# Performance work log

Hardware: AMD Instinct MI355X
Metric: run time of the kernel (lower is better)

The kernel has to match this reference:

```python
import jax, jax.numpy as jnp
import numpy as np

B, L, D, H, DH, DEPTH, VOCAB = 8, 512, 256, 8, 64, 16, 5
INNER = 4 * D  # GLU feedforward inner dim = 1024
EPS = 1e-5

def _ln(x, g, b):
    mu = jnp.mean(x, -1, keepdims=True)
    var = jnp.mean(jnp.square(x - mu), -1, keepdims=True)
    return (x - mu) * jax.lax.rsqrt(var + EPS) * g + b

def setup_inputs() -> dict:
    key = jax.random.key(0)
    ks = jax.random.split(key, 24)
    s = 0.02
    seq = jax.random.randint(ks[0], (B, L), 0, VOCAB)
    lengths = jax.random.randint(ks[1], (B,), L // 2, L + 1)
    mask = jnp.arange(L)[None, :] < lengths[:, None]  # [B, L] bool padding mask
    f32 = jnp.float32
    return {
        "seq": seq,
        "mask": mask,
        "emb": jax.random.normal(ks[2], (VOCAB, D), f32) * s,
        "png": jnp.ones((D,), f32), "pnb": jnp.zeros((D,), f32),
        "ln1g": jnp.ones((DEPTH, D), f32), "ln1b": jnp.zeros((DEPTH, D), f32),
        "Wq": jax.random.normal(ks[3], (DEPTH, D, H * DH), f32) * s,
        "Wk": jax.random.normal(ks[4], (DEPTH, D, H * DH), f32) * s,
        "Wv": jax.random.normal(ks[5], (DEPTH, D, H * DH), f32) * s,
        "Wo": jax.random.normal(ks[6], (DEPTH, H * DH, D), f32) * s,
        "ln2g": jnp.ones((DEPTH, D), f32), "ln2b": jnp.zeros((DEPTH, D), f32),
        "W1": jax.random.normal(ks[7], (DEPTH, D, 2 * INNER), f32) * s,
        "b1": jnp.zeros((DEPTH, 2 * INNER), f32),
        "W2": jax.random.normal(ks[8], (DEPTH, INNER, D), f32) * s,
        "b2": jnp.zeros((DEPTH, D), f32),
        "fng": jnp.ones((D,), f32), "fnb": jnp.zeros((D,), f32),
        "Wout": jax.random.normal(ks[9], (D, 2), f32) * s,
        "bout": jnp.zeros((2,), f32),
    }

def _alibi_bias(n):
    # heads=8 is a power of two: slopes = 2^{-1}..2^{-8}
    slopes = 2.0 ** (-(jnp.arange(1, H + 1, dtype=jnp.float32)) * (8.0 / H))
    pos = jnp.arange(n, dtype=jnp.float32)
    rel = -jnp.abs(pos[None, :] - pos[:, None])  # [n, n]
    return slopes[:, None, None] * rel  # [H, n, n]

def _forward(seq, mask, emb, png, pnb, ln1g, ln1b, Wq, Wk, Wv, Wo,
             ln2g, ln2b, W1, b1, W2, b2, fng, fnb, Wout, bout):
    x = emb[seq]                      # [B, L, D]
    x = _ln(x, png, pnb)              # post_emb_norm
    bias = _alibi_bias(L)             # [H, L, L]
    kv_mask = mask[:, None, None, :]  # [B, 1, 1, L]
    scale = DH ** -0.5

    def layer(x, p):
        (g1, c1, wq, wk, wv, wo, g2, c2, w1, bb1, w2, bb2) = p
        h = _ln(x, g1, c1)
        q = (h @ wq).reshape(B, L, H, DH).transpose(0, 2, 1, 3)  # bhld
        k = (h @ wk).reshape(B, L, H, DH).transpose(0, 2, 1, 3)
        v = (h @ wv).reshape(B, L, H, DH).transpose(0, 2, 1, 3)
        scores = jnp.einsum('bhid,bhjd->bhij', q, k) * scale + bias
        scores = jnp.where(kv_mask, scores, jnp.float32(-1e9))
        a = jax.nn.softmax(scores, axis=-1)
        o = jnp.einsum('bhij,bhjd->bhid', a, v)
        o = o.transpose(0, 2, 1, 3).reshape(B, L, H * DH) @ wo
        x = x + o
        h2 = _ln(x, g2, c2)
        u = h2 @ w1 + bb1
        val, gate = jnp.split(u, 2, axis=-1)  # GLU: x * gelu(gate)
        x = x + (val * jax.nn.gelu(gate, approximate=False)) @ w2 + bb2
        return x, None

    x, _ = jax.lax.scan(layer, x, (ln1g, ln1b, Wq, Wk, Wv, Wo, ln2g, ln2b, W1, b1, W2, b2))
    x = _ln(x, fng, fnb)              # final encoder norm
    return x @ Wout + bout            # [B, L, 2]

def reference(seq, mask, emb, png, pnb, ln1g, ln1b, Wq, Wk, Wv, Wo,
              ln2g, ln2b, W1, b1, W2, b2, fng, fnb, Wout, bout):
    return _forward(seq, mask, emb, png, pnb, ln1g, ln1b, Wq, Wk, Wv, Wo,
                    ln2g, ln2b, W1, b1, W2, b2, fng, fnb, Wout, bout)
```

## Files before the change

### kernel.cpp

```cpp
#include <hip/hip_runtime.h>
#include <cstdint>
#include <cstddef>

#define BB 8
#define LL 512
#define DD 256
#define HH 8
#define DHD 64
#define NLAYER 16
#define HDH 512
#define IN2 2048
#define IN1 1024

typedef __attribute__((ext_vector_type(8))) short short8;
typedef __attribute__((ext_vector_type(4))) float floatx4;
typedef __attribute__((ext_vector_type(4))) unsigned short ushort4v;
typedef unsigned short u16;

__device__ __forceinline__ floatx4 mfma16(short8 a, short8 b, floatx4 c) {
  return __builtin_amdgcn_mfma_f32_16x16x32_bf16(a, b, c, 0, 0, 0);
}

__device__ __forceinline__ u16 f2b(float f) {
  union { float f; unsigned u; } x; x.f = f;
  unsigned u = x.u + 0x7fffu + ((x.u >> 16) & 1u);
  return (u16)(u >> 16);
}
__device__ __forceinline__ float b2f(u16 s) {
  union { unsigned u; float f; } x; x.u = ((unsigned)s) << 16;
  return x.f;
}

__device__ __forceinline__ float wave_sum(float s) {
#pragma unroll
  for (int off = 32; off; off >>= 1) s += __shfl_xor(s, off);
  return s;
}

__device__ __forceinline__ void gload_lds16(const u16* g, u16* l) {
  __builtin_amdgcn_global_load_lds((__attribute__((address_space(1))) void*)g,
                                   (__attribute__((address_space(3))) void*)l,
                                   16, 0, 0);
}

template <int NSLOTS>
__device__ __forceinline__ void stage_tile(const u16* __restrict__ g, int rowstride,
                                           u16* lds, int tid) {
  int wave = tid >> 6, lane = tid & 63;
#pragma unroll
  for (int j = 0; j < NSLOTS / 256; ++j) {
    int sbase = j * 256 + wave * 64;
    int slot = sbase + lane;
    int row = slot >> 3;
    int kg = (slot & 7) ^ (row & 7);
    gload_lds16(g + (size_t)row * rowstride + kg * 8, lds + sbase * 8);
  }
}

__device__ __forceinline__ short8 ld_frag(const u16* T, int row, int kg) {
  return *(const short8*)&T[(row << 6) + (((kg ^ row) & 7) << 3)];
}

__device__ __forceinline__ float4 ln_math(const float* __restrict__ x,
                                          const float* __restrict__ g,
                                          const float* __restrict__ b, int t) {
  float4 v = *(const float4*)(x + t * 4);
  float s = wave_sum(v.x + v.y + v.z + v.w);
  float mu = s * (1.0f / DD);
  float dx = v.x - mu, dy = v.y - mu, dz = v.z - mu, dw = v.w - mu;
  float ss = wave_sum(dx * dx + dy * dy + dz * dz + dw * dw);
  float r = rsqrtf(ss * (1.0f / DD) + 1e-5f);
  float4 gg = *(const float4*)(g + t * 4);
  float4 bb = *(const float4*)(b + t * 4);
  float4 o;
  o.x = dx * r * gg.x + bb.x;
  o.y = dy * r * gg.y + bb.y;
  o.z = dz * r * gg.z + bb.z;
  o.w = dw * r * gg.w + bb.w;
  return o;
}

__global__ __launch_bounds__(256) void embed_ln_kernel(
    const int* __restrict__ seq, const float* __restrict__ emb,
    const float* __restrict__ png, const float* __restrict__ pnb,
    const float* __restrict__ g1, const float* __restrict__ b1,
    float* __restrict__ X, u16* __restrict__ H) {
  int row = blockIdx.x * 4 + (threadIdx.x >> 6), t = threadIdx.x & 63;
  int tok = seq[row];
  float4 o = ln_math(emb + (size_t)tok * DD, png, pnb, t);
  *(float4*)(X + (size_t)row * DD + t * 4) = o;
  float s = wave_sum(o.x + o.y + o.z + o.w);
  float mu = s * (1.0f / DD);
  float dx = o.x - mu, dy = o.y - mu, dz = o.z - mu, dw = o.w - mu;
  float ss = wave_sum(dx * dx + dy * dy + dz * dz + dw * dw);
  float r = rsqrtf(ss * (1.0f / DD) + 1e-5f);
  float4 gg = *(const float4*)(g1 + t * 4);
  float4 bb = *(const float4*)(b1 + t * 4);
  ushort4v o4;
  o4[0] = f2b(dx * r * gg.x + bb.x);
  o4[1] = f2b(dy * r * gg.y + bb.y);
  o4[2] = f2b(dz * r * gg.z + bb.z);
  o4[3] = f2b(dw * r * gg.w + bb.w);
  *(ushort4v*)(H + (size_t)row * DD + t * 4) = o4;
}

#define WBUF_LAYER 1310720
__global__ __launch_bounds__(256) void prep_weights_kernel(
    const float* __restrict__ Wq, const float* __restrict__ Wk,
    const float* __restrict__ Wv, const float* __restrict__ Wo,
    const float* __restrict__ W1, const float* __restrict__ W2,
    u16* __restrict__ wbuf_all) {
  __shared__ float tile[32][33];
  int l = blockIdx.x / 1280;
  int bx = blockIdx.x % 1280;
  int tid = threadIdx.x;
  const float* wq = Wq + (size_t)l * DD * HDH;
  const float* wk = Wk + (size_t)l * DD * HDH;
  const float* wv = Wv + (size_t)l * DD * HDH;
  const float* wo = Wo + (size_t)l * HDH * DD;
  const float* w1 = W1 + (size_t)l * DD * IN2;
  const float* w2 = W2 + (size_t)l * IN1 * DD;
  u16* wbuf = wbuf_all + (size_t)l * WBUF_LAYER;

  const float* src; int srcld; u16* dst; int dstld; int dn0, k0, scol0;
  int packW1 = 0;
  if (bx < 384) {
    int t = bx; dn0 = (t % 48) * 32; k0 = (t / 48) * 32;
    scol0 = dn0 & 511;
    src = (dn0 < 512) ? wq : ((dn0 < 1024) ? wk : wv);
    srcld = 512; dst = wbuf; dstld = 256;
  } else if (bx < 512) {
    int t = bx - 384; dn0 = (t % 8) * 32; k0 = (t / 8) * 32; scol0 = dn0;
    src = wo; srcld = 256; dst = wbuf + 393216; dstld = 512;
  } else if (bx < 1024) {
    int t = bx - 512; dn0 = (t % 64) * 32; k0 = (t / 64) * 32; scol0 = dn0;
    src = w1; srcld = 2048; dst = wbuf + 524288; dstld = 256; packW1 = 1;
  } else {
    int t = bx - 1024; dn0 = (t % 8) * 32; k0 = (t / 8) * 32; scol0 = dn0;
    src = w2; srcld = 256; dst = wbuf + 1048576; dstld = 1024;
  }
  int r = tid >> 3, c4 = (tid & 7) * 4;
  float4 v = *(const float4*)&src[(size_t)(k0 + r) * srcld + scol0 + c4];
  tile[r][c4 + 0] = v.x; tile[r][c4 + 1] = v.y;
  tile[r][c4 + 2] = v.z; tile[r][c4 + 3] = v.w;
  __syncthreads();
  int n = tid >> 3, kk = (tid & 7) * 4;
  int drow = dn0 + n;
  if (packW1) {
    if (drow < 1024) drow = ((drow >> 4) << 5) | (drow & 15);
    else { int nn = drow - 1024; drow = (((nn >> 4) << 5) + 16) | (nn & 15); }
  }
  ushort4v o4;
  o4[0] = f2b(tile[kk + 0][n]); o4[1] = f2b(tile[kk + 1][n]);
  o4[2] = f2b(tile[kk + 2][n]); o4[3] = f2b(tile[kk + 3][n]);
  *(ushort4v*)&dst[(size_t)drow * dstld + k0 + kk] = o4;
}

__global__ __launch_bounds__(256) void gemm_qkv(
    const u16* __restrict__ A, const u16* __restrict__ BT,
    u16* __restrict__ qk, u16* __restrict__ vT) {
  __shared__ __align__(16) u16 As[128 * 64];
  __shared__ __align__(16) u16 Bs[128 * 64];
  int tid = threadIdx.x;
  int wave = tid >> 6, lane = tid & 63;
  int lm = lane & 15, quad = lane >> 4;
  int wr = wave >> 1, wc = wave & 1;
  int n0 = blockIdx.x * 128, m0 = blockIdx.y * 128;

  floatx4 acc[4][4];
#pragma unroll
  for (int mf = 0; mf < 4; ++mf)
#pragma unroll
    for (int nf = 0; nf < 4; ++nf)
#pragma unroll
      for (int r = 0; r < 4; ++r) acc[mf][nf][r] = 0.0f;

  for (int k0 = 0; k0 < DD; k0 += 64) {
    __syncthreads();
    stage_tile<1024>(A + (size_t)m0 * DD + k0, DD, As, tid);
    stage_tile<1024>(BT + (size_t)n0 * DD + k0, DD, Bs, tid);
    __syncthreads();
#pragma unroll
    for (int kc = 0; kc < 2; ++kc) {
      short8 af[4], bf[4];
#pragma unroll
      for (int mf = 0; mf < 4; ++mf)
        af[mf] = ld_frag(As, wr * 64 + mf * 16 + lm, kc * 4 + quad);
#pragma unroll
      for (int nf = 0; nf < 4; ++nf)
        bf[nf] = ld_frag(Bs, wc * 64 + nf * 16 + lm, kc * 4 + quad);
#pragma unroll
      for (int mf = 0; mf < 4; ++mf)
#pragma unroll
        for (int nf = 0; nf < 4; ++nf)
          acc[mf][nf] = mfma16(af[mf], bf[nf], acc[mf][nf]);
    }
  }
  if (n0 < 1024) {
#pragma unroll
    for (int mf = 0; mf < 4; ++mf)
#pragma unroll
      for (int nf = 0; nf < 4; ++nf)
#pragma unroll
        for (int r = 0; r < 4; ++r) {
          int row = m0 + wr * 64 + mf * 16 + quad * 4 + r;
          int col = n0 + wc * 64 + nf * 16 + lm;
          qk[(size_t)row * 1024 + col] = f2b(acc[mf][nf][r]);
        }
  } else {
#pragma unroll
    for (int mf = 0; mf < 4; ++mf)
#pragma unroll
      for (int nf = 0; nf < 4; ++nf) {
        int token0 = m0 + wr * 64 + mf * 16 + quad * 4;
        int hd = n0 + wc * 64 + nf * 16 + lm - 1024;
        int b = token0 >> 9, key = token0 & 511;
        ushort4v p4;
#pragma unroll
        for (int r = 0; r < 4; ++r) p4[r] = f2b(acc[mf][nf][r]);
        *(ushort4v*)&vT[((size_t)(b * 8 + (hd >> 6)) * 64 + (hd & 63)) * 512 + key] = p4;
      }
  }
}

__global__ __launch_bounds__(256) void gemm_ffn1(
    const u16* __restrict__ A, const u16* __restrict__ BTp,
    const float* __restrict__ b1, u16* __restrict__ G) {
  __shared__ __align__(16) u16 As[128 * 64];
  __shared__ __align__(16) u16 Bs[128 * 64];
  int tid = threadIdx.x;
  int wave = tid >> 6, lane = tid & 63;
  int lm = lane & 15, quad = lane >> 4;
  int wr = wave >> 1, wc = wave & 1;
  int n0 = blockIdx.x * 128, m0 = blockIdx.y * 128;

  floatx4 acc[4][4];
#pragma unroll
  for (int mf = 0; mf < 4; ++mf)
#pragma unroll
    for (int nf = 0; nf < 4; ++nf)
#pragma unroll
      for (int r = 0; r < 4; ++r) acc[mf][nf][r] = 0.0f;

  for (int k0 = 0; k0 < DD; k0 += 64) {
    __syncthreads();
    stage_tile<1024>(A + (size_t)m0 * DD + k0, DD, As, tid);
    stage_tile<1024>(BTp + (size_t)n0 * DD + k0, DD, Bs, tid);
    __syncthreads();
#pragma unroll
    for (int kc = 0; kc < 2; ++kc) {
      short8 af[4], bf[4];
#pragma unroll
      for (int mf = 0; mf < 4; ++mf)
        af[mf] = ld_frag(As, wr * 64 + mf * 16 + lm, kc * 4 + quad);
#pragma unroll
      for (int nf = 0; nf < 4; ++nf)
        bf[nf] = ld_frag(Bs, wc * 64 + nf * 16 + lm, kc * 4 + quad);
#pragma unroll
      for (int mf = 0; mf < 4; ++mf)
#pragma unroll
        for (int nf = 0; nf < 4; ++nf)
          acc[mf][nf] = mfma16(af[mf], bf[nf], acc[mf][nf]);
    }
  }
  int p0 = (n0 + wc * 64) >> 5;
#pragma unroll
  for (int j = 0; j < 2; ++j) {
    int gcol = (p0 + j) * 16 + lm;
    float bv = b1[gcol], bg = b1[1024 + gcol];
#pragma unroll
    for (int mf = 0; mf < 4; ++mf)
#pragma unroll
      for (int r = 0; r < 4; ++r) {
        int row = m0 + wr * 64 + mf * 16 + quad * 4 + r;
        float val = acc[mf][2 * j][r] + bv;
        float gate = acc[mf][2 * j + 1][r] + bg;
        float ge = 0.5f * gate * (1.0f + erff(gate * 0.70710678118654752440f));
        G[(size_t)row * IN1 + gcol] = f2b(val * ge);
      }
  }
}

__global__ __launch_bounds__(256) void gemm_row_ln(
    const u16* __restrict__ A, int lda, const u16* __restrict__ BT, int K,
    const float* __restrict__ bias, float* __restrict__ X,
    const float* __restrict__ lng, const float* __restrict__ lnb,
    u16* __restrict__ Hout) {
  __shared__ __align__(16) u16 As[16 * 64];
  __shared__ __align__(16) u16 Bs[256 * 64];
  int tid = threadIdx.x;
  int wave = tid >> 6, lane = tid & 63;
  int lm = lane & 15, quad = lane >> 4;
  int m0 = blockIdx.x * 16;

  floatx4 acc[4];
#pragma unroll
  for (int nf = 0; nf < 4; ++nf)
#pragma unroll
    for (int r = 0; r < 4; ++r) acc[nf][r] = 0.0f;

  for (int k0 = 0; k0 < K; k0 += 64) {
    __syncthreads();
    if (wave < 2) {
      int sbase = wave * 64;
      int slot = sbase + lane;
      int row = slot >> 3;
      int kg = (slot & 7) ^ (row & 7);
      gload_lds16(A + (size_t)(m0 + row) * lda + k0 + kg * 8, As + sbase * 8);
    }
    stage_tile<2048>(BT + k0, K, Bs, tid);
    __syncthreads();
#pragma unroll
    for (int kc = 0; kc < 2; ++kc) {
      short8 af = ld_frag(As, lm, kc * 4 + quad);
#pragma unroll
      for (int nf = 0; nf < 4; ++nf) {
        short8 bf = ld_frag(Bs, wave * 64 + nf * 16 + lm, kc * 4 + quad);
        acc[nf] = mfma16(af, bf, acc[nf]);
      }
    }
  }
  __syncthreads();
  float* xs = (float*)Bs;
#pragma unroll
  for (int nf = 0; nf < 4; ++nf) {
    int col = wave * 64 + nf * 16 + lm;
    float bv = bias ? bias[col] : 0.0f;
#pragma unroll
    for (int r = 0; r < 4; ++r) {
      int row = quad * 4 + r;
      float v = acc[nf][r] + bv + X[(size_t)(m0 + row) * DD + col];
      X[(size_t)(m0 + row) * DD + col] = v;
      xs[row * DD + col] = v;
    }
  }
  __syncthreads();
  float4 gg = *(const float4*)(lng + lane * 4);
  float4 bb = *(const float4*)(lnb + lane * 4);
#pragma unroll
  for (int rr = 0; rr < 4; ++rr) {
    int row = wave * 4 + rr;
    float4 v = *(const float4*)&xs[row * DD + lane * 4];
    float s = wave_sum(v.x + v.y + v.z + v.w);
    float mu = s * (1.0f / DD);
    float dx = v.x - mu, dy = v.y - mu, dz = v.z - mu, dw = v.w - mu;
    float ss = wave_sum(dx * dx + dy * dy + dz * dz + dw * dw);
    float rc = rsqrtf(ss * (1.0f / DD) + 1e-5f);
    ushort4v o4;
    o4[0] = f2b(dx * rc * gg.x + bb.x);
    o4[1] = f2b(dy * rc * gg.y + bb.y);
    o4[2] = f2b(dz * rc * gg.z + bb.z);
    o4[3] = f2b(dw * rc * gg.w + bb.w);
    *(ushort4v*)(Hout + (size_t)(m0 + row) * DD + lane * 4) = o4;
  }
}

__global__ __launch_bounds__(256) void attn_mfma_kernel(
    const u16* __restrict__ qk, const u16* __restrict__ vT,
    const int* __restrict__ mask_raw, u16* __restrict__ O) {
  __shared__ __align__(16) u16 Ks[64 * 64];
  __shared__ __align__(16) u16 Vs[64 * 64];
  __shared__ __align__(16) u16 Ps[4][16][72];
  __shared__ __align__(16) float madd[64];

  const int tid = threadIdx.x, wave = tid >> 6, lane = tid & 63;
  const int lm = lane & 15, quad = lane >> 4;
  const int qb = blockIdx.x, h = blockIdx.y, b = blockIdx.z;
  const float slope = exp2f(-(float)(h + 1));

  int w0 = mask_raw[0];
  int mmode = (w0 == 1) ? 0 : ((w0 == 0x3f800000) ? 2 : 1);

  const int q0 = qb * 64 + wave * 16;
  const int qg = b * LL + q0;
  const float qpos = (float)(q0 + lm);

  const u16* qp = qk + (size_t)(qg + lm) * 1024 + h * 64 + quad * 8;
  short8 qf0 = *(const short8*)qp;
  short8 qf1 = *(const short8*)(qp + 32);

  floatx4 oc[4];
#pragma unroll
  for (int nf = 0; nf < 4; ++nf)
#pragma unroll
    for (int r = 0; r < 4; ++r) oc[nf][r] = 0.0f;
  float mrow = -1e30f, lrow = 0.0f;

  const int krow_base = b * LL;
  const u16* vbase = vT + (size_t)(b * 8 + h) * 64 * 512;
  for (int k0 = 0; k0 < LL; k0 += 64) {
    bool tile_valid;
    if (mmode == 0) tile_valid = mask_raw[krow_base + k0] != 0;
    else if (mmode == 1) tile_valid = ((const signed char*)mask_raw)[krow_base + k0] != 0;
    else tile_valid = ((const float*)mask_raw)[krow_base + k0] != 0.0f;
    if (!tile_valid) break;

    __syncthreads();
    stage_tile<512>(qk + (size_t)(krow_base + k0) * 1024 + 512 + h * 64, 1024, Ks, tid);
    stage_tile<512>(vbase + k0, 512, Vs, tid);
    if (tid < 64) {
      int gi = krow_base + k0 + tid;
      bool valid;
      if (mmode == 0) valid = mask_raw[gi] != 0;
      else if (mmode == 1) valid = ((const signed char*)mask_raw)[gi] != 0;
      else valid = ((const float*)mask_raw)[gi] != 0.0f;
      madd[tid] = valid ? 0.0f : -1e9f;
    }
    __syncthreads();

    float sc[4][4];
    float tmax = -3e38f;
#pragma unroll
    for (int nt = 0; nt < 4; ++nt) {
      floatx4 pc;
#pragma unroll
      for (int r = 0; r < 4; ++r) pc[r] = 0.0f;
      short8 kf0 = ld_frag(Ks, nt * 16 + lm, quad);
      short8 kf1 = ld_frag(Ks, nt * 16 + lm, 4 + quad);
      pc = mfma16(kf0, qf0, pc);
      pc = mfma16(kf1, qf1, pc);
      float4 ma = *(const float4*)&madd[nt * 16 + quad * 4];
      float kbase = (float)(k0 + nt * 16 + quad * 4);
#pragma unroll
      for (int r = 0; r < 4; ++r) {
        float s = pc[r] * 0.125f - slope * fabsf(qpos - (kbase + r)) +
                  ((const float*)&ma)[r];
        sc[nt][r] = s;
        tmax = fmaxf(tmax, s);
      }
    }
    tmax = fmaxf(tmax, __shfl_xor(tmax, 16));
    tmax = fmaxf(tmax, __shfl_xor(tmax, 32));
    float nm = fmaxf(mrow, tmax);
    float alpha = __expf(mrow - nm);
    mrow = nm;
    float rsum = 0.0f;
#pragma unroll
    for (int nt = 0; nt < 4; ++nt)
#pragma unroll
      for (int r = 0; r < 4; ++r) {
        float p = __expf(sc[nt][r] - nm);
        sc[nt][r] = p;
        rsum += p;
      }
    rsum += __shfl_xor(rsum, 16);
    rsum += __shfl_xor(rsum, 32);
    lrow = lrow * alpha + rsum;
    float av[4];
#pragma unroll
    for (int r = 0; r < 4; ++r) av[r] = __shfl(alpha, quad * 4 + r);
#pragma unroll
    for (int nf = 0; nf < 4; ++nf)
#pragma unroll
      for (int r = 0; r < 4; ++r) oc[nf][r] *= av[r];
#pragma unroll
    for (int nt = 0; nt < 4; ++nt) {
      ushort4v p4;
#pragma unroll
      for (int r = 0; r < 4; ++r) p4[r] = f2b(sc[nt][r]);
      *(ushort4v*)&Ps[wave][lm][nt * 16 + quad * 4] = p4;
    }
#pragma unroll
    for (int kc = 0; kc < 2; ++kc) {
      short8 af = *(const short8*)&Ps[wave][lm][kc * 32 + quad * 8];
#pragma unroll
      for (int nf = 0; nf < 4; ++nf) {
        short8 bv = ld_frag(Vs, nf * 16 + lm, kc * 4 + quad);
        oc[nf] = mfma16(af, bv, oc[nf]);
      }
    }
  }
  float rl = 1.0f / lrow;
  float rv[4];
#pragma unroll
  for (int r = 0; r < 4; ++r) rv[r] = __shfl(rl, quad * 4 + r);
#pragma unroll
  for (int nf = 0; nf < 4; ++nf)
#pragma unroll
    for (int r = 0; r < 4; ++r) {
      int qq = qg + quad * 4 + r;
      O[(size_t)qq * HDH + h * 64 + nf * 16 + lm] = f2b(oc[nf][r] * rv[r]);
    }
}

__global__ __launch_bounds__(256) void outproj_kernel(const u16* __restrict__ Hx,
                                                      const float* __restrict__ Wout,
                                                      const float* __restrict__ bout,
                                                      float* __restrict__ out) {
  int row = blockIdx.x * 4 + (threadIdx.x >> 6), t = threadIdx.x & 63;
  const u16* x = Hx + (size_t)row * DD;
  ushort4v v4 = *(const ushort4v*)(x + t * 4);
  float xv[4] = {b2f(v4[0]), b2f(v4[1]), b2f(v4[2]), b2f(v4[3])};
  float s0 = 0.0f, s1 = 0.0f;
#pragma unroll
  for (int i = 0; i < 4; ++i) {
    int d = t * 4 + i;
    s0 += xv[i] * Wout[d * 2 + 0];
    s1 += xv[i] * Wout[d * 2 + 1];
  }
  s0 = wave_sum(s0);
  s1 = wave_sum(s1);
  if (t == 0) {
    out[(size_t)row * 2 + 0] = s0 + bout[0];
    out[(size_t)row * 2 + 1] = s1 + bout[1];
  }
}

extern "C" void kernel_launch(void* const* d_in, const int* in_sizes, int n_in,
                              void* d_out, int out_size, void* d_ws, size_t ws_size,
                              hipStream_t stream) {
  const int* seq = (const int*)d_in[0];
  const int* mask = (const int*)d_in[1];
  const float* emb = (const float*)d_in[2];
  const float* png = (const float*)d_in[3];
  const float* pnb = (const float*)d_in[4];
  const float* ln1g = (const float*)d_in[5];
  const float* ln1b = (const float*)d_in[6];
  const float* Wq = (const float*)d_in[7];
  const float* Wk = (const float*)d_in[8];
  const float* Wv = (const float*)d_in[9];
  const float* Wo = (const float*)d_in[10];
  const float* ln2g = (const float*)d_in[11];
  const float* ln2b = (const float*)d_in[12];
  const float* W1 = (const float*)d_in[13];
  const float* b1 = (const float*)d_in[14];
  const float* W2 = (const float*)d_in[15];
  const float* b2 = (const float*)d_in[16];
  const float* fng = (const float*)d_in[17];
  const float* fnb = (const float*)d_in[18];
  const float* Wout = (const float*)d_in[19];
  const float* bout = (const float*)d_in[20];
  float* out = (float*)d_out;

  uint8_t* wsb = (uint8_t*)d_ws;
  float* x = (float*)(wsb + 0);
  u16* hb = (u16*)(wsb + 4194304);
  u16* wbuf = (u16*)(wsb + 6291456);
  u16* qk = (u16*)(wsb + 48234496);
  u16* vT = (u16*)(wsb + 56623104);
  u16* obuf = (u16*)(wsb + 60817408);
  u16* gbuf = (u16*)(wsb + 65011712);

  const int M = BB * LL;

  prep_weights_kernel<<<16 * 1280, 256, 0, stream>>>(Wq, Wk, Wv, Wo, W1, W2, wbuf);
  embed_ln_kernel<<<M / 4, 256, 0, stream>>>(seq, emb, png, pnb, ln1g, ln1b, x, hb);

  for (int l = 0; l < NLAYER; ++l) {
    u16* wl = wbuf + (size_t)l * WBUF_LAYER;

    gemm_qkv<<<dim3(1536 / 128, M / 128), 256, 0, stream>>>(hb, wl, qk, vT);

    attn_mfma_kernel<<<dim3(LL / 64, HH, BB), 256, 0, stream>>>(qk, vT, mask, obuf);

    gemm_row_ln<<<M / 16, 256, 0, stream>>>(
        obuf, HDH, wl + 393216, HDH, nullptr, x,
        ln2g + l * DD, ln2b + l * DD, hb);

    gemm_ffn1<<<dim3(IN2 / 128, M / 128), 256, 0, stream>>>(
        hb, wl + 524288, b1 + (size_t)l * IN2, gbuf);

    const float* ng = (l < NLAYER - 1) ? (ln1g + (l + 1) * DD) : fng;
    const float* nb = (l < NLAYER - 1) ? (ln1b + (l + 1) * DD) : fnb;
    gemm_row_ln<<<M / 16, 256, 0, stream>>>(
        gbuf, IN1, wl + 1048576, IN1, b2 + (size_t)l * DD, x, ng, nb, hb);
  }

  outproj_kernel<<<M / 4, 256, 0, stream>>>(hb, Wout, bout, out);

  (void)in_sizes; (void)n_in; (void)out_size; (void)ws_size;
}
```

Before: 1.331 ms.

## Double-buffer LDS tiles in GEMMs and attention, widen row-LN GEMM, fuse output projection

Converts the QKV, FFN1, row-LN GEMMs and the attention kernel to double-buffered LDS staging, so the next K tile's global-to-LDS load is issued while the current tile feeds MFMAs. This also drops one barrier per iteration. The row-LN GEMM moves to 512 threads with two fragments per wave. Attention precomputes the number of valid key tiles and applies the mask add only on the boundary tile, and the final output projection is fused into the last row-LN launch. The extra LDS use (the row-LN kernel doubles its B buffer to about 64KB) may lower occupancy. The boundary-only mask assumes a prefix padding mask.

```diff
diff --git a/kernel.cpp b/kernel.cpp
--- a/kernel.cpp
+++ b/kernel.cpp
@@ -43,13 +43,13 @@
                                    16, 0, 0);
 }
 
-template <int NSLOTS>
+template <int NSLOTS, int NTHREADS = 256>
 __device__ __forceinline__ void stage_tile(const u16* __restrict__ g, int rowstride,
                                            u16* lds, int tid) {
   int wave = tid >> 6, lane = tid & 63;
 #pragma unroll
-  for (int j = 0; j < NSLOTS / 256; ++j) {
-    int sbase = j * 256 + wave * 64;
+  for (int j = 0; j < NSLOTS / NTHREADS; ++j) {
+    int sbase = j * NTHREADS + wave * 64;
     int slot = sbase + lane;
     int row = slot >> 3;
     int kg = (slot & 7) ^ (row & 7);
@@ -159,13 +159,15 @@
 __global__ __launch_bounds__(256) void gemm_qkv(
     const u16* __restrict__ A, const u16* __restrict__ BT,
     u16* __restrict__ qk, u16* __restrict__ vT) {
-  __shared__ __align__(16) u16 As[128 * 64];
-  __shared__ __align__(16) u16 Bs[128 * 64];
+  __shared__ __align__(16) u16 As[2][128 * 64];
+  __shared__ __align__(16) u16 Bs[2][128 * 64];
   int tid = threadIdx.x;
   int wave = tid >> 6, lane = tid & 63;
   int lm = lane & 15, quad = lane >> 4;
   int wr = wave >> 1, wc = wave & 1;
   int n0 = blockIdx.x * 128, m0 = blockIdx.y * 128;
+  const u16* Ab = A + (size_t)m0 * DD;
+  const u16* Bb = BT + (size_t)n0 * DD;
 
   floatx4 acc[4][4];
 #pragma unroll
@@ -175,26 +177,33 @@
 #pragma unroll
       for (int r = 0; r < 4; ++r) acc[mf][nf][r] = 0.0f;
 
-  for (int k0 = 0; k0 < DD; k0 += 64) {
-    __syncthreads();
-    stage_tile<1024>(A + (size_t)m0 * DD + k0, DD, As, tid);
-    stage_tile<1024>(BT + (size_t)n0 * DD + k0, DD, Bs, tid);
-    __syncthreads();
+  stage_tile<1024>(Ab, DD, As[0], tid);
+  stage_tile<1024>(Bb, DD, Bs[0], tid);
+  __syncthreads();
+#pragma unroll
+  for (int it = 0; it < 4; ++it) {
+    if (it < 3) {
+      stage_tile<1024>(Ab + (it + 1) * 64, DD, As[(it + 1) & 1], tid);
+      stage_tile<1024>(Bb + (it + 1) * 64, DD, Bs[(it + 1) & 1], tid);
+    }
+    const u16* Ac = As[it & 1];
+    const u16* Bc = Bs[it & 1];
 #pragma unroll
     for (int kc = 0; kc < 2; ++kc) {
       short8 af[4], bf[4];
 #pragma unroll
       for (int mf = 0; mf < 4; ++mf)
-        af[mf] = ld_frag(As, wr * 64 + mf * 16 + lm, kc * 4 + quad);
+        af[mf] = ld_frag(Ac, wr * 64 + mf * 16 + lm, kc * 4 + quad);
 #pragma unroll
       for (int nf = 0; nf < 4; ++nf)
-        bf[nf] = ld_frag(Bs, wc * 64 + nf * 16 + lm, kc * 4 + quad);
+        bf[nf] = ld_frag(Bc, wc * 64 + nf * 16 + lm, kc * 4 + quad);
 #pragma unroll
       for (int mf = 0; mf < 4; ++mf)
 #pragma unroll
         for (int nf = 0; nf < 4; ++nf)
           acc[mf][nf] = mfma16(af[mf], bf[nf], acc[mf][nf]);
     }
+    if (it < 3) __syncthreads();
   }
   if (n0 < 1024) {
 #pragma unroll
@@ -226,13 +235,15 @@
 __global__ __launch_bounds__(256) void gemm_ffn1(
     const u16* __restrict__ A, const u16* __restrict__ BTp,
     const float* __restrict__ b1, u16* __restrict__ G) {
-  __shared__ __align__(16) u16 As[128 * 64];
-  __shared__ __align__(16) u16 Bs[128 * 64];
+  __shared__ __align__(16) u16 As[2][128 * 64];
+  __shared__ __align__(16) u16 Bs[2][128 * 64];
   int tid = threadIdx.x;
   int wave = tid >> 6, lane = tid & 63;
   int lm = lane & 15, quad = lane >> 4;
   int wr = wave >> 1, wc = wave & 1;
   int n0 = blockIdx.x * 128, m0 = blockIdx.y * 128;
+  const u16* Ab = A + (size_t)m0 * DD;
+  const u16* Bb = BTp + (size_t)n0 * DD;
 
   floatx4 acc[4][4];
 #pragma unroll
@@ -242,26 +253,33 @@
 #pragma unroll
       for (int r = 0; r < 4; ++r) acc[mf][nf][r] = 0.0f;
 
-  for (int k0 = 0; k0 < DD; k0 += 64) {
-    __syncthreads();
-    stage_tile<1024>(A + (size_t)m0 * DD + k0, DD, As, tid);
-    stage_tile<1024>(BTp + (size_t)n0 * DD + k0, DD, Bs, tid);
-    __syncthreads();
+  stage_tile<1024>(Ab, DD, As[0], tid);
+  stage_tile<1024>(Bb, DD, Bs[0], tid);
+  __syncthreads();
+#pragma unroll
+  for (int it = 0; it < 4; ++it) {
+    if (it < 3) {
+      stage_tile<1024>(Ab + (it + 1) * 64, DD, As[(it + 1) & 1], tid);
+      stage_tile<1024>(Bb + (it + 1) * 64, DD, Bs[(it + 1) & 1], tid);
+    }
+    const u16* Ac = As[it & 1];
+    const u16* Bc = Bs[it & 1];
 #pragma unroll
     for (int kc = 0; kc < 2; ++kc) {
       short8 af[4], bf[4];
 #pragma unroll
       for (int mf = 0; mf < 4; ++mf)
-        af[mf] = ld_frag(As, wr * 64 + mf * 16 + lm, kc * 4 + quad);
+        af[mf] = ld_frag(Ac, wr * 64 + mf * 16 + lm, kc * 4 + quad);
 #pragma unroll
       for (int nf = 0; nf < 4; ++nf)
-        bf[nf] = ld_frag(Bs, wc * 64 + nf * 16 + lm, kc * 4 + quad);
+        bf[nf] = ld_frag(Bc, wc * 64 + nf * 16 + lm, kc * 4 + quad);
 #pragma unroll
       for (int mf = 0; mf < 4; ++mf)
 #pragma unroll
         for (int nf = 0; nf < 4; ++nf)
           acc[mf][nf] = mfma16(af[mf], bf[nf], acc[mf][nf]);
     }
+    if (it < 3) __syncthreads();
   }
   int p0 = (n0 + wc * 64) >> 5;
 #pragma unroll
@@ -281,50 +299,63 @@
   }
 }
 
-__global__ __launch_bounds__(256) void gemm_row_ln(
+__global__ __launch_bounds__(512) void gemm_row_ln(
     const u16* __restrict__ A, int lda, const u16* __restrict__ BT, int K,
     const float* __restrict__ bias, float* __restrict__ X,
     const float* __restrict__ lng, const float* __restrict__ lnb,
-    u16* __restrict__ Hout) {
-  __shared__ __align__(16) u16 As[16 * 64];
-  __shared__ __align__(16) u16 Bs[256 * 64];
+    u16* __restrict__ Hout,
+    const float* __restrict__ Wout, const float* __restrict__ bout,
+    float* __restrict__ outp) {
+  __shared__ __align__(16) u16 As[2][16 * 64];
+  __shared__ __align__(16) u16 Bs[2][256 * 64];
   int tid = threadIdx.x;
   int wave = tid >> 6, lane = tid & 63;
   int lm = lane & 15, quad = lane >> 4;
   int m0 = blockIdx.x * 16;
 
-  floatx4 acc[4];
-#pragma unroll
-  for (int nf = 0; nf < 4; ++nf)
+  floatx4 acc[2];
+#pragma unroll
+  for (int nf = 0; nf < 2; ++nf)
 #pragma unroll
     for (int r = 0; r < 4; ++r) acc[nf][r] = 0.0f;
 
-  for (int k0 = 0; k0 < K; k0 += 64) {
-    __syncthreads();
-    if (wave < 2) {
-      int sbase = wave * 64;
-      int slot = sbase + lane;
-      int row = slot >> 3;
-      int kg = (slot & 7) ^ (row & 7);
-      gload_lds16(A + (size_t)(m0 + row) * lda + k0 + kg * 8, As + sbase * 8);
-    }
-    stage_tile<2048>(BT + k0, K, Bs, tid);
-    __syncthreads();
+  const u16* Ab = A + (size_t)m0 * lda;
+  if (wave < 2) {
+    int slot = wave * 64 + lane;
+    int row = slot >> 3, kg = (slot & 7) ^ (row & 7);
+    gload_lds16(Ab + (size_t)row * lda + kg * 8, As[0] + wave * 64 * 8);
+  }
+  stage_tile<2048, 512>(BT, K, Bs[0], tid);
+  __syncthreads();
+  int iters = K >> 6;
+  for (int it = 0; it < iters; ++it) {
+    if (it + 1 < iters) {
+      int kn = (it + 1) * 64;
+      if (wave < 2) {
+        int slot = wave * 64 + lane;
+        int row = slot >> 3, kg = (slot & 7) ^ (row & 7);
+        gload_lds16(Ab + (size_t)row * lda + kn + kg * 8,
+                    As[(it + 1) & 1] + wave * 64 * 8);
+      }
+      stage_tile<2048, 512>(BT + kn, K, Bs[(it + 1) & 1], tid);
+    }
+    const u16* Ac = As[it & 1];
+    const u16* Bc = Bs[it & 1];
 #pragma unroll
     for (int kc = 0; kc < 2; ++kc) {
-      short8 af = ld_frag(As, lm, kc * 4 + quad);
-#pragma unroll
-      for (int nf = 0; nf < 4; ++nf) {
-        short8 bf = ld_frag(Bs, wave * 64 + nf * 16 + lm, kc * 4 + quad);
+      short8 af = ld_frag(Ac, lm, kc * 4 + quad);
+#pragma unroll
+      for (int nf = 0; nf < 2; ++nf) {
+        short8 bf = ld_frag(Bc, wave * 32 + nf * 16 + lm, kc * 4 + quad);
         acc[nf] = mfma16(af, bf, acc[nf]);
       }
     }
-  }
-  __syncthreads();
-  float* xs = (float*)Bs;
-#pragma unroll
-  for (int nf = 0; nf < 4; ++nf) {
-    int col = wave * 64 + nf * 16 + lm;
+    if (it + 1 < iters) __syncthreads();
+  }
+  float* xs = (float*)Bs[0];
+#pragma unroll
+  for (int nf = 0; nf < 2; ++nf) {
+    int col = wave * 32 + nf * 16 + lm;
     float bv = bias ? bias[col] : 0.0f;
 #pragma unroll
     for (int r = 0; r < 4; ++r) {
@@ -338,28 +369,42 @@
   float4 gg = *(const float4*)(lng + lane * 4);
   float4 bb = *(const float4*)(lnb + lane * 4);
 #pragma unroll
-  for (int rr = 0; rr < 4; ++rr) {
-    int row = wave * 4 + rr;
+  for (int rr = 0; rr < 2; ++rr) {
+    int row = wave * 2 + rr;
     float4 v = *(const float4*)&xs[row * DD + lane * 4];
     float s = wave_sum(v.x + v.y + v.z + v.w);
     float mu = s * (1.0f / DD);
     float dx = v.x - mu, dy = v.y - mu, dz = v.z - mu, dw = v.w - mu;
     float ss = wave_sum(dx * dx + dy * dy + dz * dz + dw * dw);
     float rc = rsqrtf(ss * (1.0f / DD) + 1e-5f);
+    float o0 = dx * rc * gg.x + bb.x;
+    float o1 = dy * rc * gg.y + bb.y;
+    float o2 = dz * rc * gg.z + bb.z;
+    float o3 = dw * rc * gg.w + bb.w;
     ushort4v o4;
-    o4[0] = f2b(dx * rc * gg.x + bb.x);
-    o4[1] = f2b(dy * rc * gg.y + bb.y);
-    o4[2] = f2b(dz * rc * gg.z + bb.z);
-    o4[3] = f2b(dw * rc * gg.w + bb.w);
+    o4[0] = f2b(o0); o4[1] = f2b(o1); o4[2] = f2b(o2); o4[3] = f2b(o3);
     *(ushort4v*)(Hout + (size_t)(m0 + row) * DD + lane * 4) = o4;
+    if (Wout) {
+      int d0 = lane * 4;
+      float s0 = o0 * Wout[d0 * 2] + o1 * Wout[(d0 + 1) * 2] +
+                 o2 * Wout[(d0 + 2) * 2] + o3 * Wout[(d0 + 3) * 2];
+      float s1 = o0 * Wout[d0 * 2 + 1] + o1 * Wout[(d0 + 1) * 2 + 1] +
+                 o2 * Wout[(d0 + 2) * 2 + 1] + o3 * Wout[(d0 + 3) * 2 + 1];
+      s0 = wave_sum(s0);
+      s1 = wave_sum(s1);
+      if (lane == 0) {
+        outp[(size_t)(m0 + row) * 2 + 0] = s0 + bout[0];
+        outp[(size_t)(m0 + row) * 2 + 1] = s1 + bout[1];
+      }
+    }
   }
 }
 
 __global__ __launch_bounds__(256) void attn_mfma_kernel(
     const u16* __restrict__ qk, const u16* __restrict__ vT,
     const int* __restrict__ mask_raw, u16* __restrict__ O) {
-  __shared__ __align__(16) u16 Ks[64 * 64];
-  __shared__ __align__(16) u16 Vs[64 * 64];
+  __shared__ __align__(16) u16 Ks[2][64 * 64];
+  __shared__ __align__(16) u16 Vs[2][64 * 64];
   __shared__ __align__(16) u16 Ps[4][16][72];
   __shared__ __align__(16) float madd[64];
 
@@ -370,6 +415,18 @@
 
   int w0 = mask_raw[0];
   int mmode = (w0 == 1) ? 0 : ((w0 == 0x3f800000) ? 2 : 1);
+  const int krow_base = b * LL;
+
+  int ntv = 8;
+#pragma unroll
+  for (int t = 7; t >= 0; --t) {
+    bool tv;
+    int gi = krow_base + t * 64;
+    if (mmode == 0) tv = mask_raw[gi] != 0;
+    else if (mmode == 1) tv = ((const signed char*)mask_raw)[gi] != 0;
+    else tv = ((const float*)mask_raw)[gi] != 0.0f;
+    if (!tv) ntv = t;
+  }
 
   const int q0 = qb * 64 + wave * 16;
   const int qg = b * LL + q0;
@@ -386,27 +443,30 @@
     for (int r = 0; r < 4; ++r) oc[nf][r] = 0.0f;
   float mrow = -1e30f, lrow = 0.0f;
 
-  const int krow_base = b * LL;
+  const u16* kbase_p = qk + (size_t)krow_base * 1024 + 512 + h * 64;
   const u16* vbase = vT + (size_t)(b * 8 + h) * 64 * 512;
-  for (int k0 = 0; k0 < LL; k0 += 64) {
-    bool tile_valid;
-    if (mmode == 0) tile_valid = mask_raw[krow_base + k0] != 0;
-    else if (mmode == 1) tile_valid = ((const signed char*)mask_raw)[krow_base + k0] != 0;
-    else tile_valid = ((const float*)mask_raw)[krow_base + k0] != 0.0f;
-    if (!tile_valid) break;
-
-    __syncthreads();
-    stage_tile<512>(qk + (size_t)(krow_base + k0) * 1024 + 512 + h * 64, 1024, Ks, tid);
-    stage_tile<512>(vbase + k0, 512, Vs, tid);
-    if (tid < 64) {
-      int gi = krow_base + k0 + tid;
-      bool valid;
-      if (mmode == 0) valid = mask_raw[gi] != 0;
-      else if (mmode == 1) valid = ((const signed char*)mask_raw)[gi] != 0;
-      else valid = ((const float*)mask_raw)[gi] != 0.0f;
-      madd[tid] = valid ? 0.0f : -1e9f;
-    }
-    __syncthreads();
+
+  stage_tile<512>(kbase_p, 1024, Ks[0], tid);
+  stage_tile<512>(vbase, 512, Vs[0], tid);
+  if (tid < 64) {
+    int gi = krow_base + (ntv - 1) * 64 + tid;
+    bool valid;
+    if (mmode == 0) valid = mask_raw[gi] != 0;
+    else if (mmode == 1) valid = ((const signed char*)mask_raw)[gi] != 0;
+    else valid = ((const float*)mask_raw)[gi] != 0.0f;
+    madd[tid] = valid ? 0.0f : -1e9f;
+  }
+  __syncthreads();
+
+  for (int t = 0; t < ntv; ++t) {
+    int k0 = t * 64;
+    if (t + 1 < ntv) {
+      stage_tile<512>(kbase_p + (size_t)(t + 1) * 64 * 1024, 1024, Ks[(t + 1) & 1], tid);
+      stage_tile<512>(vbase + (t + 1) * 64, 512, Vs[(t + 1) & 1], tid);
+    }
+    const u16* Kc = Ks[t & 1];
+    const u16* Vc = Vs[t & 1];
+    bool bnd = (t == ntv - 1);
 
     float sc[4][4];
     float tmax = -3e38f;
@@ -415,19 +475,23 @@
       floatx4 pc;
 #pragma unroll
       for (int r = 0; r < 4; ++r) pc[r] = 0.0f;
-      short8 kf0 = ld_frag(Ks, nt * 16 + lm, quad);
-      short8 kf1 = ld_frag(Ks, nt * 16 + lm, 4 + quad);
+      short8 kf0 = ld_frag(Kc, nt * 16 + lm, quad);
+      short8 kf1 = ld_frag(Kc, nt * 16 + lm, 4 + quad);
       pc = mfma16(kf0, qf0, pc);
       pc = mfma16(kf1, qf1, pc);
-      float4 ma = *(const float4*)&madd[nt * 16 + quad * 4];
       float kbase = (float)(k0 + nt * 16 + quad * 4);
 #pragma unroll
       for (int r = 0; r < 4; ++r) {
-        float s = pc[r] * 0.125f - slope * fabsf(qpos - (kbase + r)) +
-                  ((const float*)&ma)[r];
+        float s = pc[r] * 0.125f - slope * fabsf(qpos - (kbase + r));
         sc[nt][r] = s;
-        tmax = fmaxf(tmax, s);
-      }
+      }
+      if (bnd) {
+        float4 ma = *(const float4*)&madd[nt * 16 + quad * 4];
+#pragma unroll
+        for (int r = 0; r < 4; ++r) sc[nt][r] += ((const float*)&ma)[r];
+      }
+#pragma unroll
+      for (int r = 0; r < 4; ++r) tmax = fmaxf(tmax, sc[nt][r]);
     }
     tmax = fmaxf(tmax, __shfl_xor(tmax, 16));
     tmax = fmaxf(tmax, __shfl_xor(tmax, 32));
@@ -465,10 +529,11 @@
       short8 af = *(const short8*)&Ps[wave][lm][kc * 32 + quad * 8];
 #pragma unroll
       for (int nf = 0; nf < 4; ++nf) {
-        short8 bv = ld_frag(Vs, nf * 16 + lm, kc * 4 + quad);
+        short8 bv = ld_frag(Vc, nf * 16 + lm, kc * 4 + quad);
         oc[nf] = mfma16(af, bv, oc[nf]);
       }
     }
+    if (t + 1 < ntv) __syncthreads();
   }
   float rl = 1.0f / lrow;
   float rv[4];
@@ -481,29 +546,6 @@
       int qq = qg + quad * 4 + r;
       O[(size_t)qq * HDH + h * 64 + nf * 16 + lm] = f2b(oc[nf][r] * rv[r]);
     }
-}
-
-__global__ __launch_bounds__(256) void outproj_kernel(const u16* __restrict__ Hx,
-                                                      const float* __restrict__ Wout,
-                                                      const float* __restrict__ bout,
-                                                      float* __restrict__ out) {
-  int row = blockIdx.x * 4 + (threadIdx.x >> 6), t = threadIdx.x & 63;
-  const u16* x = Hx + (size_t)row * DD;
-  ushort4v v4 = *(const ushort4v*)(x + t * 4);
-  float xv[4] = {b2f(v4[0]), b2f(v4[1]), b2f(v4[2]), b2f(v4[3])};
-  float s0 = 0.0f, s1 = 0.0f;
-#pragma unroll
-  for (int i = 0; i < 4; ++i) {
-    int d = t * 4 + i;
-    s0 += xv[i] * Wout[d * 2 + 0];
-    s1 += xv[i] * Wout[d * 2 + 1];
-  }
-  s0 = wave_sum(s0);
-  s1 = wave_sum(s1);
-  if (t == 0) {
-    out[(size_t)row * 2 + 0] = s0 + bout[0];
-    out[(size_t)row * 2 + 1] = s1 + bout[1];
-  }
 }
 
 extern "C" void kernel_launch(void* const* d_in, const int* in_sizes, int n_in,
@@ -553,20 +595,22 @@
 
     attn_mfma_kernel<<<dim3(LL / 64, HH, BB), 256, 0, stream>>>(qk, vT, mask, obuf);
 
-    gemm_row_ln<<<M / 16, 256, 0, stream>>>(
+    gemm_row_ln<<<M / 16, 512, 0, stream>>>(
         obuf, HDH, wl + 393216, HDH, nullptr, x,
-        ln2g + l * DD, ln2b + l * DD, hb);
+        ln2g + l * DD, ln2b + l * DD, hb, nullptr, nullptr, nullptr);
 
     gemm_ffn1<<<dim3(IN2 / 128, M / 128), 256, 0, stream>>>(
         hb, wl + 524288, b1 + (size_t)l * IN2, gbuf);
 
     const float* ng = (l < NLAYER - 1) ? (ln1g + (l + 1) * DD) : fng;
     const float* nb = (l < NLAYER - 1) ? (ln1b + (l + 1) * DD) : fnb;
-    gemm_row_ln<<<M / 16, 256, 0, stream>>>(
-        gbuf, IN1, wl + 1048576, IN1, b2 + (size_t)l * DD, x, ng, nb, hb);
-  }
-
-  outproj_kernel<<<M / 4, 256, 0, stream>>>(hb, Wout, bout, out);
+    const float* wo_p = (l == NLAYER - 1) ? Wout : nullptr;
+    const float* bo_p = (l == NLAYER - 1) ? bout : nullptr;
+    float* out_p = (l == NLAYER - 1) ? out : nullptr;
+    gemm_row_ln<<<M / 16, 512, 0, stream>>>(
+        gbuf, IN1, wl + 1048576, IN1, b2 + (size_t)l * DD, x, ng, nb, hb,
+        wo_p, bo_p, out_p);
+  }
 
   (void)in_sizes; (void)n_in; (void)out_size; (void)ws_size;
 }
```

New measurement: 1.280 ms. 3.9% less time.
